# Kernel optimization log

Measured on AMD Instinct MI355X. Metric: run time of the kernel, lower is better.

## Reference

```python
import jax, jax.numpy as jnp
import numpy as np

N_VARS = 8
D_MODEL = 512
L = 8192
B = 32
G = 1  # num_global_tokens
PATCH_LENS = [16, 16, 32, 32, 64, 64, 128, 128]
SAMPLING = [1, 1, 2, 2, 1, 1, 2, 2]
UNIQUE_PLS = [16, 32, 64, 128]


def _pos_emb(n, d):
    # standard sinusoidal positional embedding (Informer/Transformer style)
    pos = np.arange(n, dtype=np.float32)[:, None]
    div = np.exp(np.arange(0, d, 2, dtype=np.float32) * (-np.log(10000.0) / d))
    pe = np.zeros((n, d), dtype=np.float32)
    pe[:, 0::2] = np.sin(pos * div)
    pe[:, 1::2] = np.cos(pos * div)
    return jnp.asarray(pe)


def setup_inputs() -> dict:
    key = jax.random.key(0)
    ks = jax.random.split(key, 16)
    inp = {"x": jax.random.normal(ks[0], (B, N_VARS, L), dtype=jnp.float32)}
    # one Linear(patch_len, d_model) per unique patch_len; torch Linear weight is (out,in)
    for i, pl in enumerate(UNIQUE_PLS):
        bound = 1.0 / np.sqrt(pl)
        inp[f"w{pl}"] = jax.random.uniform(ks[1 + 2 * i], (D_MODEL, pl), minval=-bound, maxval=bound, dtype=jnp.float32)
        inp[f"b{pl}"] = jax.random.uniform(ks[2 + 2 * i], (D_MODEL,), minval=-bound, maxval=bound, dtype=jnp.float32)
    inp["glb_tokens"] = jax.random.normal(ks[10], (1, G, D_MODEL), dtype=jnp.float32)
    inp["channel_emb"] = jax.random.normal(ks[11], (N_VARS, D_MODEL), dtype=jnp.float32)
    return inp


def reference(x, w16, b16, w32, b32, w64, b64, w128, b128, glb_tokens, channel_emb):
    wdict = {16: (w16, b16), 32: (w32, b32), 64: (w64, b64), 128: (w128, b128)}
    Bn = x.shape[0]
    min_sp = min(SAMPLING)
    outs = []
    for v in range(N_VARS):
        pl = PATCH_LENS[v]
        sf = SAMPLING[v] // min_sp
        n_p = L // (pl * sf)  # num patches for this variable
        # strided gather: element j of patch i sits at i*pl*sf + j*sf -> reshape trick
        patches = x[:, v, : n_p * pl * sf].reshape(Bn, n_p, pl, sf)[..., 0]  # [B, n_p, pl]
        w, b = wdict[pl]
        emb = jnp.einsum('bnp,dp->bnd', patches, w) + b          # [B, n_p, d]
        emb = emb + _pos_emb(n_p, D_MODEL)                        # positional add
        emb = jnp.concatenate([emb, jnp.broadcast_to(glb_tokens, (Bn, G, D_MODEL))], axis=1)
        emb = emb + channel_emb[v]                                # channel add (incl. global token)
        outs.append(emb)
    return jnp.concatenate(outs, axis=1)  # [B, sum(n_p + G), d] = [32, 1608, 512]
```

## Files before the change

### kernel.cpp

```cpp
#include <hip/hip_runtime.h>
#include <math.h>

#define DM 512
#define LSEQ 8192
#define NV 8
#define TOK 1608
#define BROWS 32
#define NTHR 256

typedef _Float16 h2 __attribute__((ext_vector_type(2)));

__device__ __constant__ int c_segv[8]   = {6, 7, 4, 5, 2, 3, 0, 1};
__device__ __constant__ int c_cum[9]    = {0, 32, 64, 192, 320, 448, 576, 1088, 1600};
__device__ __constant__ int c_lgch[8]   = {0, 0, 2, 2, 2, 2, 4, 4};
__device__ __constant__ int c_tokoff[8] = {0, 513, 1026, 1155, 1284, 1413, 1542, 1575};
__device__ __constant__ int c_np[8]     = {512, 512, 128, 128, 128, 128, 32, 32};
__device__ __constant__ int c_pl[8]     = {16, 16, 32, 32, 64, 64, 128, 128};
__device__ __constant__ int c_sf[8]     = {1, 1, 2, 2, 1, 1, 2, 2};
__device__ __constant__ int c_wtoff[8]  = {262144, 262144, 266240, 266240,
                                           274432, 274432, 290816, 290816};

__device__ __forceinline__ float fdot2f(h2 a, h2 b, float c) {
#if __has_builtin(__builtin_amdgcn_fdot2)
    return __builtin_amdgcn_fdot2(a, b, c, false);
#else
    return fmaf((float)a.y, (float)b.y, fmaf((float)a.x, (float)b.x, c));
#endif
}
__device__ __forceinline__ h2 bch2(unsigned u) { return __builtin_bit_cast(h2, u); }

__global__ __launch_bounds__(512) void setup_kernel(
    const float* __restrict__ w16, const float* __restrict__ w32,
    const float* __restrict__ w64, const float* __restrict__ w128,
    float* __restrict__ ws)
{
    int bid = blockIdx.x;
    int d = threadIdx.x;
    if (bid < 512) {
        int idx = bid * 512 + d;
        int i = idx >> 9;
        int dd = idx & (DM - 1);
        const float c = -9.210340371976184f / 512.0f;
        float div = expf((float)(dd & ~1) * c);
        float ang = (float)i * div;
        ws[idx] = (dd & 1) ? cosf(ang) : sinf(ang);
        return;
    }
    int j = bid - 512;
    const float* w; int pl, k2, off;
    if (j < 8)       { w = w16;  pl = 16;  k2 = j;      off = 262144; }
    else if (j < 24) { w = w32;  pl = 32;  k2 = j - 8;  off = 266240; }
    else if (j < 56) { w = w64;  pl = 64;  k2 = j - 24; off = 274432; }
    else             { w = w128; pl = 128; k2 = j - 56; off = 290816; }
    float2 p = *reinterpret_cast<const float2*>(w + (size_t)d * pl + 2 * k2);
    h2 h; h.x = (_Float16)p.x; h.y = (_Float16)p.y;
    reinterpret_cast<unsigned*>(ws)[off + k2 * DM + d] = __builtin_bit_cast(unsigned, h);
}

__global__ __launch_bounds__(NTHR) void patch_embed_kernel(
    const float* __restrict__ x,
    const float* __restrict__ b16,  const float* __restrict__ b32,
    const float* __restrict__ b64,  const float* __restrict__ b128,
    const float* __restrict__ glb,  const float* __restrict__ chan,
    const float* __restrict__ ws,   float* __restrict__ out)
{
    extern __shared__ float ldsf[];
    unsigned* ldsu = reinterpret_cast<unsigned*>(ldsf);
    int bid = blockIdx.x;
    const int tid = threadIdx.x;

    if (bid >= 1600) {
        int v = bid - 1600;
        int d2 = tid << 1;
        float2 g = *reinterpret_cast<const float2*>(glb + d2);
        float2 c = *reinterpret_cast<const float2*>(chan + v * DM + d2);
        float2 o; o.x = g.x + c.x; o.y = g.y + c.y;
        int row0 = c_tokoff[v] + c_np[v];
        for (int b = 0; b < 32; ++b)
            *reinterpret_cast<float2*>(out + ((size_t)(b * TOK + row0)) * DM + d2) = o;
        return;
    }

    int seg = 0;
    while (bid >= c_cum[seg + 1]) ++seg;
    int local = bid - c_cum[seg];
    int v = c_segv[seg];
    int lg = c_lgch[seg];
    int b = local >> lg;
    int chunk = local & ((1 << lg) - 1);
    const int pl = c_pl[v];
    const int sf = c_sf[v];
    const int pl2 = pl >> 1;
    const int i0 = chunk * BROWS;

    const int ne2 = (BROWS * pl) >> 1;
    const float* xb = x + ((size_t)b * NV + v) * LSEQ + (size_t)i0 * (pl * sf);
    if (sf == 1) {
        for (int t = tid; t < (ne2 >> 1); t += NTHR) {
            float4 q = *reinterpret_cast<const float4*>(xb + 4 * t);
            h2 a; a.x = (_Float16)q.x; a.y = (_Float16)q.y;
            h2 c; c.x = (_Float16)q.z; c.y = (_Float16)q.w;
            uint2 o; o.x = __builtin_bit_cast(unsigned, a);
            o.y = __builtin_bit_cast(unsigned, c);
            *reinterpret_cast<uint2*>(ldsu + 2 * t) = o;
        }
    } else {
        for (int p = tid; p < ne2; p += NTHR) {
            float4 q = *reinterpret_cast<const float4*>(xb + 4 * p);
            h2 a; a.x = (_Float16)q.x; a.y = (_Float16)q.z;
            ldsu[p] = __builtin_bit_cast(unsigned, a);
        }
    }
    __syncthreads();

    const int lane = tid & 63;
    const int wv   = tid >> 6;
    const int c0   = lane << 3;
    const unsigned* prow = ldsu + (wv * 8) * pl2;
    const unsigned* wtv  = reinterpret_cast<const unsigned*>(ws) + c_wtoff[v];

    float acc[8][8];
#pragma unroll
    for (int r = 0; r < 8; ++r)
#pragma unroll
        for (int c = 0; c < 8; ++c) acc[r][c] = 0.f;

    uint4 wa0 = *reinterpret_cast<const uint4*>(wtv + c0);
    uint4 wb0 = *reinterpret_cast<const uint4*>(wtv + c0 + 4);
    uint4 wa1 = *reinterpret_cast<const uint4*>(wtv + DM + c0);
    uint4 wb1 = *reinterpret_cast<const uint4*>(wtv + DM + c0 + 4);

    for (int k2 = 0; k2 < pl2; k2 += 2) {
        uint4 na0, nb0, na1, nb1;
        if (k2 + 2 < pl2) {
            const unsigned* wn = wtv + (k2 + 2) * DM;
            na0 = *reinterpret_cast<const uint4*>(wn + c0);
            nb0 = *reinterpret_cast<const uint4*>(wn + c0 + 4);
            na1 = *reinterpret_cast<const uint4*>(wn + DM + c0);
            nb1 = *reinterpret_cast<const uint4*>(wn + DM + c0 + 4);
        }
        uint2 pr[8];
#pragma unroll
        for (int r = 0; r < 8; ++r)
            pr[r] = *reinterpret_cast<const uint2*>(prow + r * pl2 + k2);
#pragma unroll
        for (int r = 0; r < 8; ++r) {
            h2 p0 = bch2(pr[r].x);
            h2 p1 = bch2(pr[r].y);
            acc[r][0] = fdot2f(p1, bch2(wa1.x), fdot2f(p0, bch2(wa0.x), acc[r][0]));
            acc[r][1] = fdot2f(p1, bch2(wa1.y), fdot2f(p0, bch2(wa0.y), acc[r][1]));
            acc[r][2] = fdot2f(p1, bch2(wa1.z), fdot2f(p0, bch2(wa0.z), acc[r][2]));
            acc[r][3] = fdot2f(p1, bch2(wa1.w), fdot2f(p0, bch2(wa0.w), acc[r][3]));
            acc[r][4] = fdot2f(p1, bch2(wb1.x), fdot2f(p0, bch2(wb0.x), acc[r][4]));
            acc[r][5] = fdot2f(p1, bch2(wb1.y), fdot2f(p0, bch2(wb0.y), acc[r][5]));
            acc[r][6] = fdot2f(p1, bch2(wb1.z), fdot2f(p0, bch2(wb0.z), acc[r][6]));
            acc[r][7] = fdot2f(p1, bch2(wb1.w), fdot2f(p0, bch2(wb0.w), acc[r][7]));
        }
        wa0 = na0; wb0 = nb0; wa1 = na1; wb1 = nb1;
    }

    const float* bias = (pl == 16) ? b16 : (pl == 32) ? b32 : (pl == 64) ? b64 : b128;
    float4 bcA, bcB;
    {
        float4 ba = *reinterpret_cast<const float4*>(bias + c0);
        float4 bb = *reinterpret_cast<const float4*>(bias + c0 + 4);
        float4 ca = *reinterpret_cast<const float4*>(chan + v * DM + c0);
        float4 cb = *reinterpret_cast<const float4*>(chan + v * DM + c0 + 4);
        bcA.x = ba.x + ca.x; bcA.y = ba.y + ca.y; bcA.z = ba.z + ca.z; bcA.w = ba.w + ca.w;
        bcB.x = bb.x + cb.x; bcB.y = bb.y + cb.y; bcB.z = bb.z + cb.z; bcB.w = bb.w + cb.w;
    }

    const int row0 = i0 + wv * 8;
    float* ob = out + ((size_t)(b * TOK + c_tokoff[v] + row0)) * DM + c0;
    const float* pb = ws  + (size_t)row0 * DM + c0;
#pragma unroll
    for (int r = 0; r < 8; ++r) {
        float4 pA = *reinterpret_cast<const float4*>(pb + (size_t)r * DM);
        float4 pB = *reinterpret_cast<const float4*>(pb + (size_t)r * DM + 4);
        float4 oA, oB;
        oA.x = acc[r][0] + bcA.x + pA.x;
        oA.y = acc[r][1] + bcA.y + pA.y;
        oA.z = acc[r][2] + bcA.z + pA.z;
        oA.w = acc[r][3] + bcA.w + pA.w;
        oB.x = acc[r][4] + bcB.x + pB.x;
        oB.y = acc[r][5] + bcB.y + pB.y;
        oB.z = acc[r][6] + bcB.z + pB.z;
        oB.w = acc[r][7] + bcB.w + pB.w;
        *reinterpret_cast<float4*>(ob + (size_t)r * DM)     = oA;
        *reinterpret_cast<float4*>(ob + (size_t)r * DM + 4) = oB;
    }
}

extern "C" void kernel_launch(void* const* d_in, const int* in_sizes, int n_in,
                              void* d_out, int out_size, void* d_ws, size_t ws_size,
                              hipStream_t stream) {
    const float* x    = (const float*)d_in[0];
    const float* w16  = (const float*)d_in[1];
    const float* b16  = (const float*)d_in[2];
    const float* w32  = (const float*)d_in[3];
    const float* b32  = (const float*)d_in[4];
    const float* w64  = (const float*)d_in[5];
    const float* b64  = (const float*)d_in[6];
    const float* w128 = (const float*)d_in[7];
    const float* b128 = (const float*)d_in[8];
    const float* glb  = (const float*)d_in[9];
    const float* chan = (const float*)d_in[10];
    float* out = (float*)d_out;
    float* ws  = (float*)d_ws;

    hipLaunchKernelGGL(setup_kernel, dim3(632), dim3(512), 0, stream,
                       w16, w32, w64, w128, ws);
    hipLaunchKernelGGL(patch_embed_kernel, dim3(1608), dim3(NTHR),
                       BROWS * 64 * sizeof(unsigned),
                       stream,
                       x, b16, b32, b64, b128, glb, chan, ws, out);
}
```

Measured before the change: 42.84 us.

## Split output columns across two blocks per tile and use nontemporal stores

Each block now computes half of the 512 output columns (4 columns per lane instead of 8), which doubles the grid to 3208 blocks and halves per-thread accumulator registers. Launch bounds request 5 blocks per SM for higher occupancy, and the output stores become nontemporal so the large write stream bypasses cache. The cost is that each patch tile is loaded from x into LDS and converted twice, once by each of the two blocks.

After: 37.85 us. -11.6%, faster.

```diff
diff --git a/kernel.cpp b/kernel.cpp
--- a/kernel.cpp
+++ b/kernel.cpp
@@ -9,9 +9,10 @@
 #define NTHR 256
 
 typedef _Float16 h2 __attribute__((ext_vector_type(2)));
+typedef float f4n __attribute__((ext_vector_type(4)));
 
 __device__ __constant__ int c_segv[8]   = {6, 7, 4, 5, 2, 3, 0, 1};
-__device__ __constant__ int c_cum[9]    = {0, 32, 64, 192, 320, 448, 576, 1088, 1600};
+__device__ __constant__ int c_cum[9]    = {0, 64, 128, 384, 640, 896, 1152, 2176, 3200};
 __device__ __constant__ int c_lgch[8]   = {0, 0, 2, 2, 2, 2, 4, 4};
 __device__ __constant__ int c_tokoff[8] = {0, 513, 1026, 1155, 1284, 1413, 1542, 1575};
 __device__ __constant__ int c_np[8]     = {512, 512, 128, 128, 128, 128, 32, 32};
@@ -28,6 +29,15 @@
 #endif
 }
 __device__ __forceinline__ h2 bch2(unsigned u) { return __builtin_bit_cast(h2, u); }
+
+__device__ __forceinline__ void nt_store4(float* p, float4 v) {
+#if __has_builtin(__builtin_nontemporal_store)
+    f4n t; t.x = v.x; t.y = v.y; t.z = v.z; t.w = v.w;
+    __builtin_nontemporal_store(t, reinterpret_cast<f4n*>(p));
+#else
+    *reinterpret_cast<float4*>(p) = v;
+#endif
+}
 
 __global__ __launch_bounds__(512) void setup_kernel(
     const float* __restrict__ w16, const float* __restrict__ w32,
@@ -57,7 +67,7 @@
     reinterpret_cast<unsigned*>(ws)[off + k2 * DM + d] = __builtin_bit_cast(unsigned, h);
 }
 
-__global__ __launch_bounds__(NTHR) void patch_embed_kernel(
+__global__ __launch_bounds__(NTHR, 5) void patch_embed_kernel(
     const float* __restrict__ x,
     const float* __restrict__ b16,  const float* __restrict__ b32,
     const float* __restrict__ b64,  const float* __restrict__ b128,
@@ -69,8 +79,8 @@
     int bid = blockIdx.x;
     const int tid = threadIdx.x;
 
-    if (bid >= 1600) {
-        int v = bid - 1600;
+    if (bid >= 3200) {
+        int v = bid - 3200;
         int d2 = tid << 1;
         float2 g = *reinterpret_cast<const float2*>(glb + d2);
         float2 c = *reinterpret_cast<const float2*>(chan + v * DM + d2);
@@ -85,9 +95,11 @@
     while (bid >= c_cum[seg + 1]) ++seg;
     int local = bid - c_cum[seg];
     int v = c_segv[seg];
+    int h = local & 1;
+    int rest = local >> 1;
     int lg = c_lgch[seg];
-    int b = local >> lg;
-    int chunk = local & ((1 << lg) - 1);
+    int b = rest >> lg;
+    int chunk = rest & ((1 << lg) - 1);
     const int pl = c_pl[v];
     const int sf = c_sf[v];
     const int pl2 = pl >> 1;
@@ -115,29 +127,25 @@
 
     const int lane = tid & 63;
     const int wv   = tid >> 6;
-    const int c0   = lane << 3;
+    const int c0   = (h << 8) + (lane << 2);
     const unsigned* prow = ldsu + (wv * 8) * pl2;
     const unsigned* wtv  = reinterpret_cast<const unsigned*>(ws) + c_wtoff[v];
 
-    float acc[8][8];
+    float acc[8][4];
 #pragma unroll
     for (int r = 0; r < 8; ++r)
 #pragma unroll
-        for (int c = 0; c < 8; ++c) acc[r][c] = 0.f;
-
-    uint4 wa0 = *reinterpret_cast<const uint4*>(wtv + c0);
-    uint4 wb0 = *reinterpret_cast<const uint4*>(wtv + c0 + 4);
-    uint4 wa1 = *reinterpret_cast<const uint4*>(wtv + DM + c0);
-    uint4 wb1 = *reinterpret_cast<const uint4*>(wtv + DM + c0 + 4);
+        for (int c = 0; c < 4; ++c) acc[r][c] = 0.f;
+
+    uint4 w0 = *reinterpret_cast<const uint4*>(wtv + c0);
+    uint4 w1 = *reinterpret_cast<const uint4*>(wtv + DM + c0);
 
     for (int k2 = 0; k2 < pl2; k2 += 2) {
-        uint4 na0, nb0, na1, nb1;
+        uint4 n0, n1;
         if (k2 + 2 < pl2) {
             const unsigned* wn = wtv + (k2 + 2) * DM;
-            na0 = *reinterpret_cast<const uint4*>(wn + c0);
-            nb0 = *reinterpret_cast<const uint4*>(wn + c0 + 4);
-            na1 = *reinterpret_cast<const uint4*>(wn + DM + c0);
-            nb1 = *reinterpret_cast<const uint4*>(wn + DM + c0 + 4);
+            n0 = *reinterpret_cast<const uint4*>(wn + c0);
+            n1 = *reinterpret_cast<const uint4*>(wn + DM + c0);
         }
         uint2 pr[8];
 #pragma unroll
@@ -147,27 +155,21 @@
         for (int r = 0; r < 8; ++r) {
             h2 p0 = bch2(pr[r].x);
             h2 p1 = bch2(pr[r].y);
-            acc[r][0] = fdot2f(p1, bch2(wa1.x), fdot2f(p0, bch2(wa0.x), acc[r][0]));
-            acc[r][1] = fdot2f(p1, bch2(wa1.y), fdot2f(p0, bch2(wa0.y), acc[r][1]));
-            acc[r][2] = fdot2f(p1, bch2(wa1.z), fdot2f(p0, bch2(wa0.z), acc[r][2]));
-            acc[r][3] = fdot2f(p1, bch2(wa1.w), fdot2f(p0, bch2(wa0.w), acc[r][3]));
-            acc[r][4] = fdot2f(p1, bch2(wb1.x), fdot2f(p0, bch2(wb0.x), acc[r][4]));
-            acc[r][5] = fdot2f(p1, bch2(wb1.y), fdot2f(p0, bch2(wb0.y), acc[r][5]));
-            acc[r][6] = fdot2f(p1, bch2(wb1.z), fdot2f(p0, bch2(wb0.z), acc[r][6]));
-            acc[r][7] = fdot2f(p1, bch2(wb1.w), fdot2f(p0, bch2(wb0.w), acc[r][7]));
-        }
-        wa0 = na0; wb0 = nb0; wa1 = na1; wb1 = nb1;
+            acc[r][0] = fdot2f(p1, bch2(w1.x), fdot2f(p0, bch2(w0.x), acc[r][0]));
+            acc[r][1] = fdot2f(p1, bch2(w1.y), fdot2f(p0, bch2(w0.y), acc[r][1]));
+            acc[r][2] = fdot2f(p1, bch2(w1.z), fdot2f(p0, bch2(w0.z), acc[r][2]));
+            acc[r][3] = fdot2f(p1, bch2(w1.w), fdot2f(p0, bch2(w0.w), acc[r][3]));
+        }
+        w0 = n0; w1 = n1;
     }
 
     const float* bias = (pl == 16) ? b16 : (pl == 32) ? b32 : (pl == 64) ? b64 : b128;
-    float4 bcA, bcB;
+    float4 bc;
     {
         float4 ba = *reinterpret_cast<const float4*>(bias + c0);
-        float4 bb = *reinterpret_cast<const float4*>(bias + c0 + 4);
         float4 ca = *reinterpret_cast<const float4*>(chan + v * DM + c0);
-        float4 cb = *reinterpret_cast<const float4*>(chan + v * DM + c0 + 4);
-        bcA.x = ba.x + ca.x; bcA.y = ba.y + ca.y; bcA.z = ba.z + ca.z; bcA.w = ba.w + ca.w;
-        bcB.x = bb.x + cb.x; bcB.y = bb.y + cb.y; bcB.z = bb.z + cb.z; bcB.w = bb.w + cb.w;
+        bc.x = ba.x + ca.x; bc.y = ba.y + ca.y;
+        bc.z = ba.z + ca.z; bc.w = ba.w + ca.w;
     }
 
     const int row0 = i0 + wv * 8;
@@ -176,18 +178,12 @@
 #pragma unroll
     for (int r = 0; r < 8; ++r) {
         float4 pA = *reinterpret_cast<const float4*>(pb + (size_t)r * DM);
-        float4 pB = *reinterpret_cast<const float4*>(pb + (size_t)r * DM + 4);
-        float4 oA, oB;
-        oA.x = acc[r][0] + bcA.x + pA.x;
-        oA.y = acc[r][1] + bcA.y + pA.y;
-        oA.z = acc[r][2] + bcA.z + pA.z;
-        oA.w = acc[r][3] + bcA.w + pA.w;
-        oB.x = acc[r][4] + bcB.x + pB.x;
-        oB.y = acc[r][5] + bcB.y + pB.y;
-        oB.z = acc[r][6] + bcB.z + pB.z;
-        oB.w = acc[r][7] + bcB.w + pB.w;
-        *reinterpret_cast<float4*>(ob + (size_t)r * DM)     = oA;
-        *reinterpret_cast<float4*>(ob + (size_t)r * DM + 4) = oB;
+        float4 o;
+        o.x = acc[r][0] + bc.x + pA.x;
+        o.y = acc[r][1] + bc.y + pA.y;
+        o.z = acc[r][2] + bc.z + pA.z;
+        o.w = acc[r][3] + bc.w + pA.w;
+        nt_store4(ob + (size_t)r * DM, o);
     }
 }
 
@@ -210,7 +206,7 @@
 
     hipLaunchKernelGGL(setup_kernel, dim3(632), dim3(512), 0, stream,
                        w16, w32, w64, w128, ws);
-    hipLaunchKernelGGL(patch_embed_kernel, dim3(1608), dim3(NTHR),
+    hipLaunchKernelGGL(patch_embed_kernel, dim3(3208), dim3(NTHR),
                        BROWS * 64 * sizeof(unsigned),
                        stream,
                        x, b16, b32, b64, b128, glb, chan, ws, out);
```

## Halve rows per block, restructure k-loop by four, use nontemporal output stores

Applied to the files above, without the earlier changes.

Each block now covers 16 patch rows instead of 32, so the grid doubles and each wave keeps 4x8 accumulators, with launch bounds asking for 4 blocks per CU. The inner loop steps k by four with uint4 LDS reads and software-prefetched weight registers. Output writes use nontemporal stores to avoid polluting the cache. The aim is more occupancy and parallelism for the store-bound output, at the cost of more blocks each reloading weights and redoing the patch staging.

Result: slower. 57.78 us (+34.9%).

```diff
diff --git a/kernel.cpp b/kernel.cpp
--- a/kernel.cpp
+++ b/kernel.cpp
@@ -5,14 +5,15 @@
 #define LSEQ 8192
 #define NV 8
 #define TOK 1608
-#define BROWS 32
+#define BROWS 16
 #define NTHR 256
 
 typedef _Float16 h2 __attribute__((ext_vector_type(2)));
+typedef float f4n __attribute__((ext_vector_type(4)));
 
 __device__ __constant__ int c_segv[8]   = {6, 7, 4, 5, 2, 3, 0, 1};
-__device__ __constant__ int c_cum[9]    = {0, 32, 64, 192, 320, 448, 576, 1088, 1600};
-__device__ __constant__ int c_lgch[8]   = {0, 0, 2, 2, 2, 2, 4, 4};
+__device__ __constant__ int c_cum[9]    = {0, 64, 128, 384, 640, 896, 1152, 2176, 3200};
+__device__ __constant__ int c_lgch[8]   = {1, 1, 3, 3, 3, 3, 5, 5};
 __device__ __constant__ int c_tokoff[8] = {0, 513, 1026, 1155, 1284, 1413, 1542, 1575};
 __device__ __constant__ int c_np[8]     = {512, 512, 128, 128, 128, 128, 32, 32};
 __device__ __constant__ int c_pl[8]     = {16, 16, 32, 32, 64, 64, 128, 128};
@@ -28,6 +29,15 @@
 #endif
 }
 __device__ __forceinline__ h2 bch2(unsigned u) { return __builtin_bit_cast(h2, u); }
+
+__device__ __forceinline__ void nt_store4(float* p, float4 v) {
+#if __has_builtin(__builtin_nontemporal_store)
+    f4n t; t.x = v.x; t.y = v.y; t.z = v.z; t.w = v.w;
+    __builtin_nontemporal_store(t, reinterpret_cast<f4n*>(p));
+#else
+    *reinterpret_cast<float4*>(p) = v;
+#endif
+}
 
 __global__ __launch_bounds__(512) void setup_kernel(
     const float* __restrict__ w16, const float* __restrict__ w32,
@@ -57,7 +67,17 @@
     reinterpret_cast<unsigned*>(ws)[off + k2 * DM + d] = __builtin_bit_cast(unsigned, h);
 }
 
-__global__ __launch_bounds__(NTHR) void patch_embed_kernel(
+#define DOT8(r, P, X, Y)                                        \
+    acc[r][0] = fdot2f(P, bch2((X).x), acc[r][0]);              \
+    acc[r][1] = fdot2f(P, bch2((X).y), acc[r][1]);              \
+    acc[r][2] = fdot2f(P, bch2((X).z), acc[r][2]);              \
+    acc[r][3] = fdot2f(P, bch2((X).w), acc[r][3]);              \
+    acc[r][4] = fdot2f(P, bch2((Y).x), acc[r][4]);              \
+    acc[r][5] = fdot2f(P, bch2((Y).y), acc[r][5]);              \
+    acc[r][6] = fdot2f(P, bch2((Y).z), acc[r][6]);              \
+    acc[r][7] = fdot2f(P, bch2((Y).w), acc[r][7]);
+
+__global__ __launch_bounds__(NTHR, 4) void patch_embed_kernel(
     const float* __restrict__ x,
     const float* __restrict__ b16,  const float* __restrict__ b32,
     const float* __restrict__ b64,  const float* __restrict__ b128,
@@ -69,8 +89,8 @@
     int bid = blockIdx.x;
     const int tid = threadIdx.x;
 
-    if (bid >= 1600) {
-        int v = bid - 1600;
+    if (bid >= 3200) {
+        int v = bid - 3200;
         int d2 = tid << 1;
         float2 g = *reinterpret_cast<const float2*>(glb + d2);
         float2 c = *reinterpret_cast<const float2*>(chan + v * DM + d2);
@@ -116,47 +136,49 @@
     const int lane = tid & 63;
     const int wv   = tid >> 6;
     const int c0   = lane << 3;
-    const unsigned* prow = ldsu + (wv * 8) * pl2;
+    const unsigned* prow = ldsu + (wv * 4) * pl2;
     const unsigned* wtv  = reinterpret_cast<const unsigned*>(ws) + c_wtoff[v];
 
-    float acc[8][8];
+    float acc[4][8];
 #pragma unroll
-    for (int r = 0; r < 8; ++r)
+    for (int r = 0; r < 4; ++r)
 #pragma unroll
         for (int c = 0; c < 8; ++c) acc[r][c] = 0.f;
 
-    uint4 wa0 = *reinterpret_cast<const uint4*>(wtv + c0);
-    uint4 wb0 = *reinterpret_cast<const uint4*>(wtv + c0 + 4);
-    uint4 wa1 = *reinterpret_cast<const uint4*>(wtv + DM + c0);
-    uint4 wb1 = *reinterpret_cast<const uint4*>(wtv + DM + c0 + 4);
-
-    for (int k2 = 0; k2 < pl2; k2 += 2) {
-        uint4 na0, nb0, na1, nb1;
-        if (k2 + 2 < pl2) {
-            const unsigned* wn = wtv + (k2 + 2) * DM;
-            na0 = *reinterpret_cast<const uint4*>(wn + c0);
-            nb0 = *reinterpret_cast<const uint4*>(wn + c0 + 4);
-            na1 = *reinterpret_cast<const uint4*>(wn + DM + c0);
-            nb1 = *reinterpret_cast<const uint4*>(wn + DM + c0 + 4);
+    uint4 aX0 = *reinterpret_cast<const uint4*>(wtv + c0);
+    uint4 aY0 = *reinterpret_cast<const uint4*>(wtv + c0 + 4);
+    uint4 aX1 = *reinterpret_cast<const uint4*>(wtv + DM + c0);
+    uint4 aY1 = *reinterpret_cast<const uint4*>(wtv + DM + c0 + 4);
+
+    for (int k4 = 0; k4 < pl2; k4 += 4) {
+        const unsigned* wb_ = wtv + (size_t)(k4 + 2) * DM;
+        uint4 bX0 = *reinterpret_cast<const uint4*>(wb_ + c0);
+        uint4 bY0 = *reinterpret_cast<const uint4*>(wb_ + c0 + 4);
+        uint4 bX1 = *reinterpret_cast<const uint4*>(wb_ + DM + c0);
+        uint4 bY1 = *reinterpret_cast<const uint4*>(wb_ + DM + c0 + 4);
+
+        uint4 pr0 = *reinterpret_cast<const uint4*>(prow + 0 * pl2 + k4);
+        uint4 pr1 = *reinterpret_cast<const uint4*>(prow + 1 * pl2 + k4);
+        uint4 pr2 = *reinterpret_cast<const uint4*>(prow + 2 * pl2 + k4);
+        uint4 pr3 = *reinterpret_cast<const uint4*>(prow + 3 * pl2 + k4);
+
+        DOT8(0, bch2(pr0.x), aX0, aY0)  DOT8(0, bch2(pr0.y), aX1, aY1)
+        DOT8(1, bch2(pr1.x), aX0, aY0)  DOT8(1, bch2(pr1.y), aX1, aY1)
+        DOT8(2, bch2(pr2.x), aX0, aY0)  DOT8(2, bch2(pr2.y), aX1, aY1)
+        DOT8(3, bch2(pr3.x), aX0, aY0)  DOT8(3, bch2(pr3.y), aX1, aY1)
+
+        if (k4 + 4 < pl2) {
+            const unsigned* wa_ = wtv + (size_t)(k4 + 4) * DM;
+            aX0 = *reinterpret_cast<const uint4*>(wa_ + c0);
+            aY0 = *reinterpret_cast<const uint4*>(wa_ + c0 + 4);
+            aX1 = *reinterpret_cast<const uint4*>(wa_ + DM + c0);
+            aY1 = *reinterpret_cast<const uint4*>(wa_ + DM + c0 + 4);
         }
-        uint2 pr[8];
-#pragma unroll
-        for (int r = 0; r < 8; ++r)
-            pr[r] = *reinterpret_cast<const uint2*>(prow + r * pl2 + k2);
-#pragma unroll
-        for (int r = 0; r < 8; ++r) {
-            h2 p0 = bch2(pr[r].x);
-            h2 p1 = bch2(pr[r].y);
-            acc[r][0] = fdot2f(p1, bch2(wa1.x), fdot2f(p0, bch2(wa0.x), acc[r][0]));
-            acc[r][1] = fdot2f(p1, bch2(wa1.y), fdot2f(p0, bch2(wa0.y), acc[r][1]));
-            acc[r][2] = fdot2f(p1, bch2(wa1.z), fdot2f(p0, bch2(wa0.z), acc[r][2]));
-            acc[r][3] = fdot2f(p1, bch2(wa1.w), fdot2f(p0, bch2(wa0.w), acc[r][3]));
-            acc[r][4] = fdot2f(p1, bch2(wb1.x), fdot2f(p0, bch2(wb0.x), acc[r][4]));
-            acc[r][5] = fdot2f(p1, bch2(wb1.y), fdot2f(p0, bch2(wb0.y), acc[r][5]));
-            acc[r][6] = fdot2f(p1, bch2(wb1.z), fdot2f(p0, bch2(wb0.z), acc[r][6]));
-            acc[r][7] = fdot2f(p1, bch2(wb1.w), fdot2f(p0, bch2(wb0.w), acc[r][7]));
-        }
-        wa0 = na0; wb0 = nb0; wa1 = na1; wb1 = nb1;
+
+        DOT8(0, bch2(pr0.z), bX0, bY0)  DOT8(0, bch2(pr0.w), bX1, bY1)
+        DOT8(1, bch2(pr1.z), bX0, bY0)  DOT8(1, bch2(pr1.w), bX1, bY1)
+        DOT8(2, bch2(pr2.z), bX0, bY0)  DOT8(2, bch2(pr2.w), bX1, bY1)
+        DOT8(3, bch2(pr3.z), bX0, bY0)  DOT8(3, bch2(pr3.w), bX1, bY1)
     }
 
     const float* bias = (pl == 16) ? b16 : (pl == 32) ? b32 : (pl == 64) ? b64 : b128;
@@ -170,11 +192,11 @@
         bcB.x = bb.x + cb.x; bcB.y = bb.y + cb.y; bcB.z = bb.z + cb.z; bcB.w = bb.w + cb.w;
     }
 
-    const int row0 = i0 + wv * 8;
+    const int row0 = i0 + wv * 4;
     float* ob = out + ((size_t)(b * TOK + c_tokoff[v] + row0)) * DM + c0;
     const float* pb = ws  + (size_t)row0 * DM + c0;
 #pragma unroll
-    for (int r = 0; r < 8; ++r) {
+    for (int r = 0; r < 4; ++r) {
         float4 pA = *reinterpret_cast<const float4*>(pb + (size_t)r * DM);
         float4 pB = *reinterpret_cast<const float4*>(pb + (size_t)r * DM + 4);
         float4 oA, oB;
@@ -186,8 +208,8 @@
         oB.y = acc[r][5] + bcB.y + pB.y;
         oB.z = acc[r][6] + bcB.z + pB.z;
         oB.w = acc[r][7] + bcB.w + pB.w;
-        *reinterpret_cast<float4*>(ob + (size_t)r * DM)     = oA;
-        *reinterpret_cast<float4*>(ob + (size_t)r * DM + 4) = oB;
+        nt_store4(ob + (size_t)r * DM,     oA);
+        nt_store4(ob + (size_t)r * DM + 4, oB);
     }
 }
 
@@ -210,7 +232,7 @@
 
     hipLaunchKernelGGL(setup_kernel, dim3(632), dim3(512), 0, stream,
                        w16, w32, w64, w128, ws);
-    hipLaunchKernelGGL(patch_embed_kernel, dim3(1608), dim3(NTHR),
+    hipLaunchKernelGGL(patch_embed_kernel, dim3(3208), dim3(NTHR),
                        BROWS * 64 * sizeof(unsigned),
                        stream,
                        x, b16, b32, b64, b128, glb, chan, ws, out);
```
